# Kernel optimization log

Hardware: AMD Instinct MI355X
Metric: run time of the kernel (lower is better)

## Reference

```python
import jax, jax.numpy as jnp
import numpy as np

N = 524288   # total nodes
B = 16384    # num graphs
D = 64       # node feature dim
STEPS = 2    # set2set processing steps


def _lin_params(key, out_dim, in_dim):
    k1, k2 = jax.random.split(key)
    s = 1.0 / np.sqrt(in_dim)
    W = jax.random.uniform(k1, (out_dim, in_dim), jnp.float32, -s, s)
    b = jax.random.uniform(k2, (out_dim,), jnp.float32, -s, s)
    return W, b


def setup_inputs() -> dict:
    key = jax.random.key(0)
    ks = jax.random.split(key, 16)
    inp = {}
    inp["features"] = jax.random.normal(ks[0], (N, D), jnp.float32)
    inp["batch_index"] = jnp.sort(jax.random.randint(ks[1], (N,), 0, B, dtype=jnp.int64))
    inp["eps_gate"] = jax.random.uniform(ks[2], (N, 1), jnp.float32)
    inp["noise"] = jax.random.uniform(ks[3], (N, D), jnp.float32)
    # compressor: Linear(64,64) -> BatchNorm1d(64) -> ReLU -> Linear(64,1)
    inp["c_w1"], inp["c_b1"] = _lin_params(ks[4], D, D)
    inp["bn_g"] = jnp.ones((D,), jnp.float32)
    inp["bn_b"] = jnp.zeros((D,), jnp.float32)
    inp["c_w2"], inp["c_b2"] = _lin_params(ks[5], 1, D)
    # set2set LSTM: input 2D, hidden D (gate order i,f,g,o)
    s = 1.0 / np.sqrt(D)
    inp["lstm_wih"] = jax.random.uniform(ks[6], (4 * D, 2 * D), jnp.float32, -s, s)
    inp["lstm_whh"] = jax.random.uniform(ks[7], (4 * D, D), jnp.float32, -s, s)
    inp["lstm_bih"] = jax.random.uniform(ks[8], (4 * D,), jnp.float32, -s, s)
    inp["lstm_bhh"] = jax.random.uniform(ks[9], (4 * D,), jnp.float32, -s, s)
    # predictor: 128->256->128->64
    inp["p_w1"], inp["p_b1"] = _lin_params(ks[10], 256, 2 * D)
    inp["p_w2"], inp["p_b2"] = _lin_params(ks[11], 128, 256)
    inp["p_w3"], inp["p_b3"] = _lin_params(ks[12], 64, 128)
    return inp


def _forward(features, batch_index, eps_gate, noise,
             c_w1, c_b1, bn_g, bn_b, c_w2, c_b2,
             lstm_wih, lstm_whh, lstm_bih, lstm_bhh,
             p_w1, p_b1, p_w2, p_b2, p_w3, p_b3):
    idx = batch_index
    seg_sum = lambda v: jax.ops.segment_sum(v, idx, num_segments=B)

    # ---- compressor (BatchNorm in training mode: batch stats, biased var) ----
    h = features @ c_w1.T + c_b1                       # [N, D]
    mu = h.mean(axis=0)
    var = ((h - mu) ** 2).mean(axis=0)
    h = (h - mu) * jax.lax.rsqrt(var + 1e-5) * bn_g + bn_b
    h = jax.nn.relu(h)
    p = h @ c_w2.T + c_b2                              # [N, 1]

    # ---- concrete gate ----
    bias = 1e-4
    eps = (bias - (1.0 - bias)) * eps_gate + (1.0 - bias)   # uniform in (bias, 1-bias)
    gate_inputs = jnp.log(eps) - jnp.log(1.0 - eps)
    lambda_pos = jax.nn.sigmoid(gate_inputs + p)       # [N, 1] (temperature = 1)
    lambda_neg = 1.0 - lambda_pos
    preserve_rate = (jax.nn.sigmoid(p) > 0.5).astype(jnp.float32).mean()

    # ---- per-graph mean / unbiased std of detached features ----
    static = jax.lax.stop_gradient(features)
    counts = seg_sum(jnp.ones((N,), jnp.float32))       # [B]
    mean_g = seg_sum(static) / jnp.maximum(counts, 1.0)[:, None]   # [B, D]
    diff = static - mean_g[idx]
    var_g = seg_sum(diff * diff) / jnp.maximum(counts - 1.0, 1.0)[:, None]
    std_g = jnp.sqrt(var_g)                             # [B, D]
    node_mean = mean_g[idx]                             # [N, D]
    node_std = std_g[idx]                               # [N, D]

    # ---- noisy reparameterization ----
    noisy_mean = lambda_pos * features + lambda_neg * node_mean
    noisy_std = lambda_neg * node_std
    noisy = noisy_mean + noise * noisy_std              # [N, D]

    # ---- Set2Set readout ----
    q_star = jnp.zeros((B, 2 * D), jnp.float32)
    hh = jnp.zeros((B, D), jnp.float32)
    cc = jnp.zeros((B, D), jnp.float32)
    for _ in range(STEPS):
        gates = q_star @ lstm_wih.T + hh @ lstm_whh.T + lstm_bih + lstm_bhh
        i, f, g, o = jnp.split(gates, 4, axis=-1)
        cc = jax.nn.sigmoid(f) * cc + jax.nn.sigmoid(i) * jnp.tanh(g)
        hh = jax.nn.sigmoid(o) * jnp.tanh(cc)
        q = hh                                          # [B, D]
        e = jnp.sum(noisy * q[idx], axis=-1)            # [N]
        m = jax.ops.segment_max(e, idx, num_segments=B)
        w = jnp.exp(e - m[idx])
        denom = seg_sum(w)
        a = w / denom[idx]                              # segment softmax
        r = seg_sum(a[:, None] * noisy)                 # [B, D]
        q_star = jnp.concatenate([q, r], axis=-1)

    # ---- KL ----
    epsl = 1e-7
    t1 = 0.5 * seg_sum(jnp.mean(noisy_std ** 2 / (node_std + epsl) ** 2, axis=1))[:, None]
    t2 = seg_sum(((noisy_mean - node_mean) / (node_std + epsl)) ** 2)
    KL_Loss = jnp.mean(t1 + t2)

    # ---- predictor ----
    z = jax.nn.relu(q_star @ p_w1.T + p_b1)
    z = jax.nn.relu(z @ p_w2.T + p_b2)
    predictions = z @ p_w3.T + p_b3                     # [B, 64]
    return predictions, KL_Loss, preserve_rate, lambda_pos


def reference(features, batch_index, eps_gate, noise,
              c_w1, c_b1, bn_g, bn_b, c_w2, c_b2,
              lstm_wih, lstm_whh, lstm_bih, lstm_bhh,
              p_w1, p_b1, p_w2, p_b2, p_w3, p_b3):
    return _forward(features, batch_index, eps_gate, noise,
                    c_w1, c_b1, bn_g, bn_b, c_w2, c_b2,
                    lstm_wih, lstm_whh, lstm_bih, lstm_bhh,
                    p_w1, p_b1, p_w2, p_b2, p_w3, p_b3)
```

## Files before the change

### kernel.cpp

```cpp
#include <hip/hip_runtime.h>
#include <math.h>

#define N_TOT 524288
#define B_GR  16384
#define CAPR  64

#define LOG2E 1.44269504088896f
#define LN2   0.69314718055995f

__device__ __forceinline__ float fexp2(float x) { return __builtin_amdgcn_exp2f(x); }
__device__ __forceinline__ float flog2(float x) { return __builtin_amdgcn_logf(x); }
__device__ __forceinline__ float frcp(float x)  { return __builtin_amdgcn_rcpf(x); }
__device__ __forceinline__ float sigf(float x)  { return frcp(1.0f + fexp2(-x * LOG2E)); }

__device__ __forceinline__ unsigned int f2bf(float x) {
  unsigned int u = __float_as_uint(x);
  return (u + 0x7FFFu + ((u >> 16) & 1u)) >> 16;
}
__device__ __forceinline__ float bf2f(unsigned int s) {
  return __uint_as_float(s << 16);
}

template <int CTRL>
__device__ __forceinline__ float dppadd(float v) {
  return v + __int_as_float(__builtin_amdgcn_update_dpp(
      0, __float_as_int(v), CTRL, 0xF, 0xF, true));
}
__device__ __forceinline__ float wave_red(float v) {
  v = dppadd<0x111>(v);
  v = dppadd<0x112>(v);
  v = dppadd<0x114>(v);
  v = dppadd<0x118>(v);
  v = dppadd<0x142>(v);
  v = dppadd<0x143>(v);
  return __int_as_float(__builtin_amdgcn_readlane(__float_as_int(v), 63));
}

__device__ __forceinline__ float wave_sum(float v) {
#pragma unroll
  for (int o = 32; o > 0; o >>= 1) v += __shfl_xor(v, o);
  return v;
}

__device__ __forceinline__ void load_A64(const float* __restrict__ A, size_t lda, int n0, int k0,
                                         float (*As)[68], int tid) {
#pragma unroll
  for (int s = 0; s < 4; s++) {
    int e4 = tid * 4 + s * 1024;
    int r = e4 >> 6, k = e4 & 63;
    *(float4*)&As[r][k] = *(const float4*)&A[(size_t)(n0 + r) * lda + k0 + k];
  }
}
__device__ __forceinline__ void mm64(const float (*As)[68], const float (*Wt)[68],
                                     int ty, int tx, float acc[4][4]) {
#pragma unroll
  for (int k4 = 0; k4 < 64; k4 += 4) {
    float4 b0 = *(const float4*)&Wt[k4 + 0][tx * 4];
    float4 b1 = *(const float4*)&Wt[k4 + 1][tx * 4];
    float4 b2 = *(const float4*)&Wt[k4 + 2][tx * 4];
    float4 b3 = *(const float4*)&Wt[k4 + 3][tx * 4];
#pragma unroll
    for (int i = 0; i < 4; i++) {
      float4 a = *(const float4*)&As[ty * 4 + i][k4];
      acc[i][0] = fmaf(a.w, b3.x, fmaf(a.z, b2.x, fmaf(a.y, b1.x, fmaf(a.x, b0.x, acc[i][0]))));
      acc[i][1] = fmaf(a.w, b3.y, fmaf(a.z, b2.y, fmaf(a.y, b1.y, fmaf(a.x, b0.y, acc[i][1]))));
      acc[i][2] = fmaf(a.w, b3.z, fmaf(a.z, b2.z, fmaf(a.y, b1.z, fmaf(a.x, b0.z, acc[i][2]))));
      acc[i][3] = fmaf(a.w, b3.w, fmaf(a.z, b2.w, fmaf(a.y, b1.w, fmaf(a.x, b0.w, acc[i][3]))));
    }
  }
}

__global__ void k_offsets(const int* __restrict__ idx, int* __restrict__ off) {
  int b = blockIdx.x * blockDim.x + threadIdx.x;
  if (b > B_GR) return;
  if (b == B_GR) { off[B_GR] = N_TOT; return; }
  int lo = 0, hi = N_TOT;
  while (lo < hi) { int mid = (lo + hi) >> 1; if (idx[mid] < b) lo = mid + 1; else hi = mid; }
  off[b] = lo;
}

__global__ void k_prep(const float* __restrict__ w1, const float* __restrict__ pw1,
                       const float* __restrict__ pw2, const float* __restrict__ pw3,
                       const float* __restrict__ wih,
                       float* __restrict__ w1T, float* __restrict__ pw1T,
                       float* __restrict__ pw2T, float* __restrict__ pw3T,
                       float* __restrict__ rtg) {
  int t = blockIdx.x * 256 + threadIdx.x;
  for (int i = t; i < 64 * 64; i += 16384)  { int r = i >> 6, c = i & 63;  w1T[c * 64 + r]   = w1[i]; }
  for (int i = t; i < 256 * 128; i += 16384){ int r = i >> 7, c = i & 127; pw1T[c * 256 + r] = pw1[i]; }
  for (int i = t; i < 128 * 256; i += 16384){ int r = i >> 8, c = i & 255; pw2T[c * 128 + r] = pw2[i]; }
  for (int i = t; i < 64 * 128; i += 16384) { int r = i >> 7, c = i & 127; pw3T[c * 64 + r]  = pw3[i]; }
  for (int i = t; i < 64 * 64 * 4; i += 16384) {
    int k = i >> 8, rem = i & 255, d = rem >> 2, j = rem & 3;
    rtg[i] = wih[(size_t)(j * 64 + d) * 128 + 64 + k];
  }
}

__global__ __launch_bounds__(256) void k_bn_stats(const float* __restrict__ X, const float* __restrict__ W1T,
                                                  const float* __restrict__ b1, unsigned short* __restrict__ h,
                                                  float* __restrict__ pSum, float* __restrict__ pSq) {
  __shared__ float As[64][68];
  __shared__ float Wt[64][68];
  int tid = threadIdx.x, ty = tid >> 4, tx = tid & 15;
  int n0 = blockIdx.x * 64;
  float acc[4][4] = {};
  load_A64(X, 64, n0, 0, As, tid);
  load_A64(W1T, 64, 0, 0, Wt, tid);
  __syncthreads();
  mm64(As, Wt, ty, tx, acc);
  float4 bv = *(const float4*)&b1[tx * 4];
  float cs[4] = {0, 0, 0, 0}, cq[4] = {0, 0, 0, 0};
#pragma unroll
  for (int i = 0; i < 4; i++) {
    float h0 = acc[i][0] + bv.x, h1 = acc[i][1] + bv.y;
    float h2 = acc[i][2] + bv.z, h3 = acc[i][3] + bv.w;
    ushort4 hb;
    hb.x = (unsigned short)f2bf(h0); hb.y = (unsigned short)f2bf(h1);
    hb.z = (unsigned short)f2bf(h2); hb.w = (unsigned short)f2bf(h3);
    *(ushort4*)&h[(size_t)(n0 + ty * 4 + i) * 64 + tx * 4] = hb;
    cs[0] += h0; cq[0] = fmaf(h0, h0, cq[0]);
    cs[1] += h1; cq[1] = fmaf(h1, h1, cq[1]);
    cs[2] += h2; cq[2] = fmaf(h2, h2, cq[2]);
    cs[3] += h3; cq[3] = fmaf(h3, h3, cq[3]);
  }
  __syncthreads();
  float* red = &As[0][0];
#pragma unroll
  for (int j = 0; j < 4; j++) {
    red[ty * 64 + tx * 4 + j] = cs[j];
    red[1024 + ty * 64 + tx * 4 + j] = cq[j];
  }
  __syncthreads();
  if (tid < 64) {
    float s = 0, q = 0;
#pragma unroll
    for (int t = 0; t < 16; t++) { s += red[t * 64 + tid]; q += red[1024 + t * 64 + tid]; }
    pSum[(size_t)blockIdx.x * 64 + tid] = s;
    pSq[(size_t)blockIdx.x * 64 + tid] = q;
  }
}

__global__ __launch_bounds__(256) void k_bn_final(const float* __restrict__ pSum, const float* __restrict__ pSq,
                                                  const float* __restrict__ bn_g, const float* __restrict__ bn_b,
                                                  float* __restrict__ aff) {
  int c = blockIdx.x;
  float s = 0, q = 0;
  for (int i = threadIdx.x; i < 8192; i += 256) {
    s += pSum[(size_t)i * 64 + c];
    q += pSq[(size_t)i * 64 + c];
  }
  __shared__ float rs[256], rq[256];
  rs[threadIdx.x] = s; rq[threadIdx.x] = q;
  __syncthreads();
  for (int st = 128; st > 0; st >>= 1) {
    if (threadIdx.x < st) { rs[threadIdx.x] += rs[threadIdx.x + st]; rq[threadIdx.x] += rq[threadIdx.x + st]; }
    __syncthreads();
  }
  if (threadIdx.x == 0) {
    float mu = rs[0] / (float)N_TOT;
    float var = rq[0] / (float)N_TOT - mu * mu;
    var = fmaxf(var, 0.0f);
    float A = bn_g[c] * rsqrtf(var + 1e-5f);
    aff[c] = A;
    aff[64 + c] = bn_b[c] - mu * A;
  }
}

__global__ __launch_bounds__(256) void k_lstm1(const float* __restrict__ bih, const float* __restrict__ bhh,
                                               const float* __restrict__ wih, const float* __restrict__ whh,
                                               float* __restrict__ q1, float* __restrict__ c1, float* __restrict__ sh2) {
  __shared__ float g1[256];
  __shared__ float q1s[64];
  int tid = threadIdx.x;
  g1[tid] = bih[tid] + bhh[tid];
  __syncthreads();
  if (tid < 64) {
    float ig = sigf(g1[tid]);
    float gg = tanhf(g1[128 + tid]);
    float cc = ig * gg;
    float og = sigf(g1[192 + tid]);
    float qv = og * tanhf(cc);
    q1s[tid] = qv; q1[tid] = qv; c1[tid] = cc;
  }
  __syncthreads();
  float acc = g1[tid];
  for (int k = 0; k < 64; k++)
    acc = fmaf(wih[(size_t)tid * 128 + k] + whh[(size_t)tid * 64 + k], q1s[k], acc);
  sh2[tid] = acc;
}

__global__ __launch_bounds__(256) void k_gate_h(const unsigned short* __restrict__ h, const float* __restrict__ aff,
                                                const float* __restrict__ w2, const float* __restrict__ cb2,
                                                const float* __restrict__ eps_gate,
                                                float* __restrict__ lamWS, float* __restrict__ lamOut,
                                                int* __restrict__ presPart) {
  __shared__ float Hs[64][65];
  __shared__ float A2s[64], C2s[64], w2s[64];
  __shared__ int pcnt[4];
  int tid = threadIdx.x;
  if (tid < 64) { A2s[tid] = aff[tid]; C2s[tid] = aff[64 + tid]; w2s[tid] = w2[tid]; }
  int n0 = blockIdx.x * 64;
#pragma unroll
  for (int s = 0; s < 4; s++) {
    int e4 = tid * 4 + s * 1024;
    int r = e4 >> 6, c = e4 & 63;
    ushort4 v = *(const ushort4*)&h[(size_t)(n0 + r) * 64 + c];
    Hs[r][c] = bf2f(v.x); Hs[r][c + 1] = bf2f(v.y);
    Hs[r][c + 2] = bf2f(v.z); Hs[r][c + 3] = bf2f(v.w);
  }
  __syncthreads();
  int r = tid >> 2, q = tid & 3;
  float p = 0.f;
#pragma unroll
  for (int j = 0; j < 16; j++) {
    int d = q * 16 + j;
    p = fmaf(fmaxf(fmaf(Hs[r][d], A2s[d], C2s[d]), 0.f), w2s[d], p);
  }
  p += __shfl_xor(p, 1);
  p += __shfl_xor(p, 2);
  p += cb2[0];
  unsigned long long m = __ballot(q == 0 && p > 0.0f);
  if ((tid & 63) == 0) pcnt[tid >> 6] = (int)__popcll(m);
  if (q == 0) {
    int row = n0 + r;
    float eg = eps_gate[row];
    float eps = 0.9999f - 0.9998f * eg;
    float gi = (flog2(eps) - flog2(1.0f - eps)) * LN2;
    float lam = sigf(gi + p);
    lamWS[row] = lam;
    lamOut[row] = lam;
  }
  __syncthreads();
  if (tid == 0) presPart[blockIdx.x] = pcnt[0] + pcnt[1] + pcnt[2] + pcnt[3];
}

__global__ __launch_bounds__(256) void k_graph_reg(const float* __restrict__ X, const float* __restrict__ noise,
                                                   const float* __restrict__ lam, const int* __restrict__ off,
                                                   const float* __restrict__ q1g, const float* __restrict__ c1g,
                                                   const float* __restrict__ sh2g, const float* __restrict__ rtg,
                                                   unsigned short* __restrict__ noisyFB, float* __restrict__ qstar,
                                                   float* __restrict__ klp) {
  int wg = blockIdx.x * 4 + (threadIdx.x >> 6);
  int lane = threadIdx.x & 63;
  int n0 = off[wg], cnt = off[wg + 1] - n0;
  const float THR = 8.f;
  const float* xp = X + (size_t)n0 * 64 + lane;
  const float* zp = noise + (size_t)n0 * 64 + lane;
  float r1v = 0.f;
  bool fits = (cnt <= CAPR);
  unsigned int pk[CAPR / 2];

  if (cnt > 0 && fits) {
    float s0 = 0.f, q0 = 0.f, s1 = 0.f, q1_ = 0.f;
#pragma unroll
    for (int np = 0; np < CAPR / 2; np++) {
      int n = 2 * np;
      if (n < cnt) {
        float a = xp[(size_t)n * 64];
        s0 += a; q0 = fmaf(a, a, q0);
        float b = 0.f;
        if (n + 1 < cnt) {
          b = xp[(size_t)(n + 1) * 64];
          s1 += b; q1_ = fmaf(b, b, q1_);
        }
        pk[np] = (f2bf(b) << 16) | f2bf(a);
      }
    }
    float c = (float)cnt;
    float mean = (s0 + s1) / c;
    float var = fmaxf(((q0 + q1_) - c * mean * mean) / fmaxf(c - 1.f, 1.f), 0.f);
    float sd = sqrtf(var);
    float inv = frcp(sd + 1e-7f);
    float S1 = wave_red(sd * sd * inv * inv);
    float q1v2 = q1g[lane] * LOG2E;
    float t2acc = 0.f, sumOm2 = 0.f;
    float m0 = -INFINITY, l0 = 0.f, r0 = 0.f;
    float m1 = -INFINITY, l1 = 0.f, r1a = 0.f;
#pragma unroll
    for (int np = 0; np < CAPR / 2; np++) {
      int n = 2 * np;
      if (n < cnt) {
        bool hasB = (n + 1 < cnt);
        unsigned int p2 = pk[np];
        float xA = bf2f(p2 & 0xffffu), xB = bf2f(p2 >> 16);
        float lamA = lam[n0 + n];
        float zA = zp[(size_t)n * 64];
        float lamB = hasB ? lam[n0 + n + 1] : 0.f;
        float zB = hasB ? zp[(size_t)(n + 1) * 64] : 0.f;
        float omA = 1.f - lamA, omB = 1.f - lamB;
        float nvA = fmaf(lamA, xA, omA * mean) + zA * (omA * sd);
        float nvB = fmaf(lamB, xB, omB * mean) + zB * (omB * sd);
        pk[np] = (f2bf(nvB) << 16) | f2bf(nvA);
        float ldA = lamA * (xA - mean) * inv; t2acc = fmaf(ldA, ldA, t2acc);
        sumOm2 = fmaf(omA, omA, sumOm2);
        if (hasB) {
          float ldB = lamB * (xB - mean) * inv; t2acc = fmaf(ldB, ldB, t2acc);
          sumOm2 = fmaf(omB, omB, sumOm2);
        }
        float e0 = wave_red(nvA * q1v2);
        float e1 = hasB ? wave_red(nvB * q1v2) : 0.f;
        if (e0 > m0 + THR) { float sc = fexp2(m0 - e0); l0 *= sc; r0 *= sc; m0 = e0; }
        float pA = fexp2(e0 - m0); l0 += pA; r0 = fmaf(pA, nvA, r0);
        if (hasB) {
          if (e1 > m1 + THR) { float sc = fexp2(m1 - e1); l1 *= sc; r1a *= sc; m1 = e1; }
          float pB = fexp2(e1 - m1); l1 += pB; r1a = fmaf(pB, nvB, r1a);
        }
      }
    }
    float M = fmaxf(m0, m1);
    float sc0 = fexp2(m0 - M), sc1 = (m1 == -INFINITY) ? 0.f : fexp2(m1 - M);
    float L = l0 * sc0 + l1 * sc1;
    float R = r0 * sc0 + r1a * sc1;
    r1v = R / L;
    float t2tot = wave_red(t2acc);
    if (lane == 0) klp[wg] = fmaf(0.5f * sumOm2, S1, t2tot);
  } else if (cnt > 0) {
    unsigned short* nw = noisyFB + (size_t)n0 * 64 + lane;
    float s0 = 0.f, q0 = 0.f;
    for (int n = 0; n < cnt; n++) { float a = xp[(size_t)n * 64]; s0 += a; q0 = fmaf(a, a, q0); }
    float c = (float)cnt;
    float mean = s0 / c;
    float var = fmaxf((q0 - c * mean * mean) / fmaxf(c - 1.f, 1.f), 0.f);
    float sd = sqrtf(var);
    float inv = frcp(sd + 1e-7f);
    float S1 = wave_red(sd * sd * inv * inv);
    float q1v2 = q1g[lane] * LOG2E;
    float t2acc = 0.f, sumOm2 = 0.f;
    float m0 = -INFINITY, l0 = 0.f, r0 = 0.f;
    for (int n = 0; n < cnt; n++) {
      float lamA = lam[n0 + n];
      float xA = xp[(size_t)n * 64];
      float zA = zp[(size_t)n * 64];
      float omA = 1.f - lamA;
      float nvA = fmaf(lamA, xA, omA * mean) + zA * (omA * sd);
      nw[(size_t)n * 64] = (unsigned short)f2bf(nvA);
      float ldA = lamA * (xA - mean) * inv; t2acc = fmaf(ldA, ldA, t2acc);
      sumOm2 = fmaf(omA, omA, sumOm2);
      float e0 = wave_red(nvA * q1v2);
      if (e0 > m0 + THR) { float sc = fexp2(m0 - e0); l0 *= sc; r0 *= sc; m0 = e0; }
      float pA = fexp2(e0 - m0); l0 += pA; r0 = fmaf(pA, nvA, r0);
    }
    r1v = r0 / l0;
    float t2tot = wave_red(t2acc);
    if (lane == 0) klp[wg] = fmaf(0.5f * sumOm2, S1, t2tot);
  } else {
    if (lane == 0) klp[wg] = 0.0f;
  }

  float a0 = 0.f, a1 = 0.f, a2 = 0.f, a3 = 0.f;
  const float4* rt = (const float4*)rtg;
#pragma unroll 4
  for (int k = 0; k < 64; k++) {
    float rk = __shfl(r1v, k);
    float4 w = rt[k * 64 + lane];
    a0 = fmaf(w.x, rk, a0); a1 = fmaf(w.y, rk, a1);
    a2 = fmaf(w.z, rk, a2); a3 = fmaf(w.w, rk, a3);
  }
  float ig = a0 + sh2g[lane];
  float fg = a1 + sh2g[64 + lane];
  float gg = a2 + sh2g[128 + lane];
  float og = a3 + sh2g[192 + lane];
  float c2 = sigf(fg) * c1g[lane] + sigf(ig) * tanhf(gg);
  float q2 = sigf(og) * tanhf(c2);
  qstar[(size_t)wg * 128 + lane] = q2;

  float r2v = 0.f;
  if (cnt > 0) {
    float q2v2 = q2 * LOG2E;
    float m0 = -INFINITY, l0 = 0.f, r0 = 0.f;
    float m1 = -INFINITY, l1 = 0.f, r1a = 0.f;
    if (fits) {
#pragma unroll
      for (int np = 0; np < CAPR / 2; np++) {
        int n = 2 * np;
        if (n < cnt) {
          bool hasB = (n + 1 < cnt);
          unsigned int p2 = pk[np];
          float nvA = bf2f(p2 & 0xffffu), nvB = bf2f(p2 >> 16);
          float e0 = wave_red(nvA * q2v2);
          float e1 = hasB ? wave_red(nvB * q2v2) : 0.f;
          if (e0 > m0 + THR) { float sc = fexp2(m0 - e0); l0 *= sc; r0 *= sc; m0 = e0; }
          float pA = fexp2(e0 - m0); l0 += pA; r0 = fmaf(pA, nvA, r0);
          if (hasB) {
            if (e1 > m1 + THR) { float sc = fexp2(m1 - e1); l1 *= sc; r1a *= sc; m1 = e1; }
            float pB = fexp2(e1 - m1); l1 += pB; r1a = fmaf(pB, nvB, r1a);
          }
        }
      }
    } else {
      const unsigned short* np_ = noisyFB + (size_t)n0 * 64 + lane;
      for (int n = 0; n < cnt; n++) {
        float nvA = bf2f(np_[(size_t)n * 64]);
        float e0 = wave_red(nvA * q2v2);
        if (e0 > m0 + THR) { float sc = fexp2(m0 - e0); l0 *= sc; r0 *= sc; m0 = e0; }
        float pA = fexp2(e0 - m0); l0 += pA; r0 = fmaf(pA, nvA, r0);
      }
    }
    float M = fmaxf(m0, m1);
    float sc0 = fexp2(m0 - M), sc1 = (m1 == -INFINITY) ? 0.f : fexp2(m1 - M);
    float L = l0 * sc0 + l1 * sc1;
    float R = r0 * sc0 + r1a * sc1;
    r2v = R / L;
  }
  qstar[(size_t)wg * 128 + 64 + lane] = r2v;
}

template <int KDIM, int ODIM, bool RELU>
__global__ __launch_bounds__(256) void k_linear(const float* __restrict__ A, const float* __restrict__ WT,
                                                const float* __restrict__ bias, float* __restrict__ C) {
  __shared__ float As[64][68];
  __shared__ float Wt[64][68];
  int tid = threadIdx.x, ty = tid >> 4, tx = tid & 15;
  int n0 = blockIdx.x * 64, c0 = blockIdx.y * 64;
  float acc[4][4] = {};
  for (int kt = 0; kt < KDIM; kt += 64) {
    __syncthreads();
    load_A64(A, KDIM, n0, kt, As, tid);
    load_A64(WT, ODIM, kt, c0, Wt, tid);
    __syncthreads();
    mm64(As, Wt, ty, tx, acc);
  }
#pragma unroll
  for (int i = 0; i < 4; i++) {
    int row = n0 + ty * 4 + i;
    float4 o;
    float v0 = acc[i][0] + bias[c0 + tx * 4 + 0];
    float v1 = acc[i][1] + bias[c0 + tx * 4 + 1];
    float v2 = acc[i][2] + bias[c0 + tx * 4 + 2];
    float v3 = acc[i][3] + bias[c0 + tx * 4 + 3];
    if (RELU) { v0 = fmaxf(v0, 0.f); v1 = fmaxf(v1, 0.f); v2 = fmaxf(v2, 0.f); v3 = fmaxf(v3, 0.f); }
    o.x = v0; o.y = v1; o.z = v2; o.w = v3;
    *(float4*)&C[(size_t)row * ODIM + c0 + tx * 4] = o;
  }
}

__global__ __launch_bounds__(256) void k_final(const float* __restrict__ klp, const int* __restrict__ presPart,
                                               float* __restrict__ out) {
  __shared__ float red[256];
  __shared__ int redi[256];
  float s = 0.0f;
  int pc = 0;
  for (int i = threadIdx.x; i < B_GR; i += 256) s += klp[i];
  for (int i = threadIdx.x; i < 8192; i += 256) pc += presPart[i];
  red[threadIdx.x] = s;
  redi[threadIdx.x] = pc;
  __syncthreads();
  for (int st = 128; st > 0; st >>= 1) {
    if (threadIdx.x < st) {
      red[threadIdx.x] += red[threadIdx.x + st];
      redi[threadIdx.x] += redi[threadIdx.x + st];
    }
    __syncthreads();
  }
  if (threadIdx.x == 0) {
    out[(size_t)B_GR * 64] = red[0] / (float)(B_GR * 64);
    out[(size_t)B_GR * 64 + 1] = (float)redi[0] / (float)N_TOT;
  }
}

extern "C" void kernel_launch(void* const* d_in, const int* in_sizes, int n_in,
                              void* d_out, int out_size, void* d_ws, size_t ws_size,
                              hipStream_t stream) {
  const float* features = (const float*)d_in[0];
  const int*   bidx     = (const int*)d_in[1];
  const float* eps_gate = (const float*)d_in[2];
  const float* noise    = (const float*)d_in[3];
  const float* c_w1 = (const float*)d_in[4];
  const float* c_b1 = (const float*)d_in[5];
  const float* bn_g = (const float*)d_in[6];
  const float* bn_b = (const float*)d_in[7];
  const float* c_w2 = (const float*)d_in[8];
  const float* c_b2 = (const float*)d_in[9];
  const float* wih  = (const float*)d_in[10];
  const float* whh  = (const float*)d_in[11];
  const float* bih  = (const float*)d_in[12];
  const float* bhh  = (const float*)d_in[13];
  const float* p_w1 = (const float*)d_in[14];
  const float* p_b1 = (const float*)d_in[15];
  const float* p_w2 = (const float*)d_in[16];
  const float* p_b2 = (const float*)d_in[17];
  const float* p_w3 = (const float*)d_in[18];
  const float* p_b3 = (const float*)d_in[19];
  float* out = (float*)d_out;

  float* wsf   = (float*)d_ws;
  int*   offp  = (int*)wsf;
  float* pSum  = wsf + 16448;
  float* pSq   = pSum + 524288;
  float* aff   = pSq + 524288;
  float* q1w   = aff + 128;
  float* c1w   = q1w + 64;
  float* sh2w  = c1w + 64;
  float* lamw  = sh2w + 256;
  float* cw1T  = lamw + (size_t)N_TOT;
  float* pw1T  = cw1T + 4096;
  float* pw2T  = pw1T + 32768;
  float* pw3T  = pw2T + 32768;
  float* rtgw  = pw3T + 8192;
  float* hwf   = rtgw + 16384;
  unsigned short* hb = (unsigned short*)hwf;
  unsigned short* noisyFB = hb;
  float* qstarw = hwf + (size_t)N_TOT * 64;
  float* z1w    = qstarw + (size_t)B_GR * 128;
  float* z2w    = z1w + (size_t)B_GR * 256;
  float* klpw   = z2w + (size_t)B_GR * 128;
  int*   presPart = (int*)(klpw + B_GR);

  float* lamOut = out + (size_t)B_GR * 64 + 2;

  k_offsets<<<(B_GR + 1 + 255) / 256, 256, 0, stream>>>(bidx, offp);
  k_prep<<<64, 256, 0, stream>>>(c_w1, p_w1, p_w2, p_w3, wih, cw1T, pw1T, pw2T, pw3T, rtgw);
  k_bn_stats<<<N_TOT / 64, 256, 0, stream>>>(features, cw1T, c_b1, hb, pSum, pSq);
  k_bn_final<<<64, 256, 0, stream>>>(pSum, pSq, bn_g, bn_b, aff);
  k_lstm1<<<1, 256, 0, stream>>>(bih, bhh, wih, whh, q1w, c1w, sh2w);
  k_gate_h<<<N_TOT / 64, 256, 0, stream>>>(hb, aff, c_w2, c_b2, eps_gate, lamw, lamOut, presPart);
  k_graph_reg<<<B_GR / 4, 256, 0, stream>>>(features, noise, lamw, offp, q1w, c1w, sh2w, rtgw,
                                            noisyFB, qstarw, klpw);
  k_linear<128, 256, true><<<dim3(B_GR / 64, 4), 256, 0, stream>>>(qstarw, pw1T, p_b1, z1w);
  k_linear<256, 128, true><<<dim3(B_GR / 64, 2), 256, 0, stream>>>(z1w, pw2T, p_b2, z2w);
  k_linear<128, 64, false><<<dim3(B_GR / 64, 1), 256, 0, stream>>>(z2w, pw3T, p_b3, out);
  k_final<<<1, 256, 0, stream>>>(klpw, presPart, out);
}
```

Baseline: 317.5 us.

## Use bf16 MFMA for compressor first linear layer in BN stats kernel

```diff
diff --git a/kernel.cpp b/kernel.cpp
--- a/kernel.cpp
+++ b/kernel.cpp
@@ -7,6 +7,9 @@
 
 #define LOG2E 1.44269504088896f
 #define LN2   0.69314718055995f
+
+typedef __attribute__((ext_vector_type(8))) short bf16x8;
+typedef __attribute__((ext_vector_type(4))) float f32x4;
 
 __device__ __forceinline__ float fexp2(float x) { return __builtin_amdgcn_exp2f(x); }
 __device__ __forceinline__ float flog2(float x) { return __builtin_amdgcn_logf(x); }
@@ -36,12 +39,6 @@
   return __int_as_float(__builtin_amdgcn_readlane(__float_as_int(v), 63));
 }
 
-__device__ __forceinline__ float wave_sum(float v) {
-#pragma unroll
-  for (int o = 32; o > 0; o >>= 1) v += __shfl_xor(v, o);
-  return v;
-}
-
 __device__ __forceinline__ void load_A64(const float* __restrict__ A, size_t lda, int n0, int k0,
                                          float (*As)[68], int tid) {
 #pragma unroll
@@ -82,11 +79,10 @@
 __global__ void k_prep(const float* __restrict__ w1, const float* __restrict__ pw1,
                        const float* __restrict__ pw2, const float* __restrict__ pw3,
                        const float* __restrict__ wih,
-                       float* __restrict__ w1T, float* __restrict__ pw1T,
-                       float* __restrict__ pw2T, float* __restrict__ pw3T,
-                       float* __restrict__ rtg) {
+                       float* __restrict__ pw1T, float* __restrict__ pw2T,
+                       float* __restrict__ pw3T, float* __restrict__ rtg,
+                       unsigned short* __restrict__ wfragb) {
   int t = blockIdx.x * 256 + threadIdx.x;
-  for (int i = t; i < 64 * 64; i += 16384)  { int r = i >> 6, c = i & 63;  w1T[c * 64 + r]   = w1[i]; }
   for (int i = t; i < 256 * 128; i += 16384){ int r = i >> 7, c = i & 127; pw1T[c * 256 + r] = pw1[i]; }
   for (int i = t; i < 128 * 256; i += 16384){ int r = i >> 8, c = i & 255; pw2T[c * 128 + r] = pw2[i]; }
   for (int i = t; i < 64 * 128; i += 16384) { int r = i >> 7, c = i & 127; pw3T[c * 64 + r]  = pw3[i]; }
@@ -94,47 +90,75 @@
     int k = i >> 8, rem = i & 255, d = rem >> 2, j = rem & 3;
     rtg[i] = wih[(size_t)(j * 64 + d) * 128 + 64 + k];
   }
-}
-
-__global__ __launch_bounds__(256) void k_bn_stats(const float* __restrict__ X, const float* __restrict__ W1T,
+  for (int i = t; i < 8 * 64 * 8; i += 16384) {
+    int f = i >> 9, lane = (i >> 3) & 63, j = i & 7;
+    int ct = f >> 1, kh = f & 1;
+    int k = kh * 32 + (lane >> 4) * 8 + j;
+    int col = ct * 16 + (lane & 15);
+    wfragb[i] = (unsigned short)f2bf(w1[(size_t)col * 64 + k]);
+  }
+}
+
+__global__ __launch_bounds__(256) void k_bn_stats(const float* __restrict__ X,
+                                                  const unsigned short* __restrict__ wfragb,
                                                   const float* __restrict__ b1, unsigned short* __restrict__ h,
                                                   float* __restrict__ pSum, float* __restrict__ pSq) {
-  __shared__ float As[64][68];
-  __shared__ float Wt[64][68];
-  int tid = threadIdx.x, ty = tid >> 4, tx = tid & 15;
+  __shared__ float redS[16][64];
+  __shared__ float redQ[16][64];
+  int tid = threadIdx.x, w = tid >> 6, l = tid & 63;
   int n0 = blockIdx.x * 64;
-  float acc[4][4] = {};
-  load_A64(X, 64, n0, 0, As, tid);
-  load_A64(W1T, 64, 0, 0, Wt, tid);
-  __syncthreads();
-  mm64(As, Wt, ty, tx, acc);
-  float4 bv = *(const float4*)&b1[tx * 4];
-  float cs[4] = {0, 0, 0, 0}, cq[4] = {0, 0, 0, 0};
-#pragma unroll
-  for (int i = 0; i < 4; i++) {
-    float h0 = acc[i][0] + bv.x, h1 = acc[i][1] + bv.y;
-    float h2 = acc[i][2] + bv.z, h3 = acc[i][3] + bv.w;
-    ushort4 hb;
-    hb.x = (unsigned short)f2bf(h0); hb.y = (unsigned short)f2bf(h1);
-    hb.z = (unsigned short)f2bf(h2); hb.w = (unsigned short)f2bf(h3);
-    *(ushort4*)&h[(size_t)(n0 + ty * 4 + i) * 64 + tx * 4] = hb;
-    cs[0] += h0; cq[0] = fmaf(h0, h0, cq[0]);
-    cs[1] += h1; cq[1] = fmaf(h1, h1, cq[1]);
-    cs[2] += h2; cq[2] = fmaf(h2, h2, cq[2]);
-    cs[3] += h3; cq[3] = fmaf(h3, h3, cq[3]);
-  }
-  __syncthreads();
-  float* red = &As[0][0];
-#pragma unroll
-  for (int j = 0; j < 4; j++) {
-    red[ty * 64 + tx * 4 + j] = cs[j];
-    red[1024 + ty * 64 + tx * 4 + j] = cq[j];
+  int r0 = w * 16;
+  int arow = n0 + r0 + (l & 15);
+  int kb = (l >> 4) * 8;
+  const float* xr = X + (size_t)arow * 64 + kb;
+  float4 a00 = *(const float4*)&xr[0];
+  float4 a01 = *(const float4*)&xr[4];
+  float4 a10 = *(const float4*)&xr[32];
+  float4 a11 = *(const float4*)&xr[36];
+  bf16x8 A0, A1;
+  A0[0] = (short)f2bf(a00.x); A0[1] = (short)f2bf(a00.y); A0[2] = (short)f2bf(a00.z); A0[3] = (short)f2bf(a00.w);
+  A0[4] = (short)f2bf(a01.x); A0[5] = (short)f2bf(a01.y); A0[6] = (short)f2bf(a01.z); A0[7] = (short)f2bf(a01.w);
+  A1[0] = (short)f2bf(a10.x); A1[1] = (short)f2bf(a10.y); A1[2] = (short)f2bf(a10.z); A1[3] = (short)f2bf(a10.w);
+  A1[4] = (short)f2bf(a11.x); A1[5] = (short)f2bf(a11.y); A1[6] = (short)f2bf(a11.z); A1[7] = (short)f2bf(a11.w);
+  const bf16x8* wf = (const bf16x8*)wfragb;
+  f32x4 acc0 = {0.f, 0.f, 0.f, 0.f}, acc1 = acc0, acc2 = acc0, acc3 = acc0;
+  {
+    bf16x8 B00 = wf[0 * 64 + l], B01 = wf[1 * 64 + l];
+    bf16x8 B10 = wf[2 * 64 + l], B11 = wf[3 * 64 + l];
+    bf16x8 B20 = wf[4 * 64 + l], B21 = wf[5 * 64 + l];
+    bf16x8 B30 = wf[6 * 64 + l], B31 = wf[7 * 64 + l];
+    acc0 = __builtin_amdgcn_mfma_f32_16x16x32_bf16(A0, B00, acc0, 0, 0, 0);
+    acc0 = __builtin_amdgcn_mfma_f32_16x16x32_bf16(A1, B01, acc0, 0, 0, 0);
+    acc1 = __builtin_amdgcn_mfma_f32_16x16x32_bf16(A0, B10, acc1, 0, 0, 0);
+    acc1 = __builtin_amdgcn_mfma_f32_16x16x32_bf16(A1, B11, acc1, 0, 0, 0);
+    acc2 = __builtin_amdgcn_mfma_f32_16x16x32_bf16(A0, B20, acc2, 0, 0, 0);
+    acc2 = __builtin_amdgcn_mfma_f32_16x16x32_bf16(A1, B21, acc2, 0, 0, 0);
+    acc3 = __builtin_amdgcn_mfma_f32_16x16x32_bf16(A0, B30, acc3, 0, 0, 0);
+    acc3 = __builtin_amdgcn_mfma_f32_16x16x32_bf16(A1, B31, acc3, 0, 0, 0);
+  }
+  int c16 = l & 15, rgrp = l >> 4;
+  int slot = w * 4 + rgrp;
+#pragma unroll
+  for (int ct = 0; ct < 4; ct++) {
+    f32x4 acc = (ct == 0) ? acc0 : (ct == 1) ? acc1 : (ct == 2) ? acc2 : acc3;
+    int col = ct * 16 + c16;
+    float bb = b1[col];
+    float cs = 0.f, cq = 0.f;
+#pragma unroll
+    for (int j = 0; j < 4; j++) {
+      float hv = acc[j] + bb;
+      int row = n0 + r0 + rgrp * 4 + j;
+      h[(size_t)row * 64 + col] = (unsigned short)f2bf(hv);
+      cs += hv; cq = fmaf(hv, hv, cq);
+    }
+    redS[slot][col] = cs;
+    redQ[slot][col] = cq;
   }
   __syncthreads();
   if (tid < 64) {
-    float s = 0, q = 0;
-#pragma unroll
-    for (int t = 0; t < 16; t++) { s += red[t * 64 + tid]; q += red[1024 + t * 64 + tid]; }
+    float s = 0.f, q = 0.f;
+#pragma unroll
+    for (int t = 0; t < 16; t++) { s += redS[t][tid]; q += redQ[t][tid]; }
     pSum[(size_t)blockIdx.x * 64 + tid] = s;
     pSq[(size_t)blockIdx.x * 64 + tid] = q;
   }
@@ -492,12 +516,12 @@
   float* c1w   = q1w + 64;
   float* sh2w  = c1w + 64;
   float* lamw  = sh2w + 256;
-  float* cw1T  = lamw + (size_t)N_TOT;
-  float* pw1T  = cw1T + 4096;
+  float* pw1T  = lamw + (size_t)N_TOT;
   float* pw2T  = pw1T + 32768;
   float* pw3T  = pw2T + 32768;
   float* rtgw  = pw3T + 8192;
-  float* hwf   = rtgw + 16384;
+  unsigned short* wfragb = (unsigned short*)(rtgw + 16384);
+  float* hwf   = rtgw + 16384 + 2048;
   unsigned short* hb = (unsigned short*)hwf;
   unsigned short* noisyFB = hb;
   float* qstarw = hwf + (size_t)N_TOT * 64;
@@ -509,8 +533,8 @@
   float* lamOut = out + (size_t)B_GR * 64 + 2;
 
   k_offsets<<<(B_GR + 1 + 255) / 256, 256, 0, stream>>>(bidx, offp);
-  k_prep<<<64, 256, 0, stream>>>(c_w1, p_w1, p_w2, p_w3, wih, cw1T, pw1T, pw2T, pw3T, rtgw);
-  k_bn_stats<<<N_TOT / 64, 256, 0, stream>>>(features, cw1T, c_b1, hb, pSum, pSq);
+  k_prep<<<64, 256, 0, stream>>>(c_w1, p_w1, p_w2, p_w3, wih, pw1T, pw2T, pw3T, rtgw, wfragb);
+  k_bn_stats<<<N_TOT / 64, 256, 0, stream>>>(features, wfragb, c_b1, hb, pSum, pSq);
   k_bn_final<<<64, 256, 0, stream>>>(pSum, pSq, bn_g, bn_b, aff);
   k_lstm1<<<1, 256, 0, stream>>>(bih, bhh, wih, whh, q1w, c1w, sh2w);
   k_gate_h<<<N_TOT / 64, 256, 0, stream>>>(hb, aff, c_w2, c_b2, eps_gate, lamw, lamOut, presPart);
```

New measurement: 292.1 us. -8.0%, faster.
